# Kernel tuning notes

Hardware: AMD Instinct MI355X
Metric: run time of the kernel (lower is better)

## Reference

```python
import jax, jax.numpy as jnp
import numpy as np

B, T, EEG, GEO, TH, HID, OUT = 4096, 320, 64, 18, 32, 16, 4
THETA0, BETA, TAU_A, TAU_M, EPS = 0.5, 1.8, 0.36, 0.8, 1e-5


@jax.custom_vjp
def spike_fn(x):
    return jnp.where(x >= 0, 1.0, 0.0).astype(x.dtype)

def _spike_fwd(x):
    return spike_fn(x), x

def _spike_bwd(x, g):
    # SuperSpike-style surrogate gradient (original defvjp not shown in source)
    return (g / (10.0 * jnp.abs(x) + 1.0) ** 2,)

spike_fn.defvjp(_spike_fwd, _spike_bwd)


def setup_inputs() -> dict:
    key = jax.random.key(0)
    ks = jax.random.split(key, 20)
    rn = lambda k, s, sc=0.05: (jax.random.normal(k, s, jnp.float32) * sc)
    return {
        "x_eeg": jax.random.normal(ks[0], (B, T, EEG), jnp.float32),
        "x_geo": jax.random.normal(ks[1], (B, T, GEO), jnp.float32),
        "conv1_k": rn(ks[2], (5, EEG, TH)),   # (W, Cin, Cout)
        "conv1_b": jnp.zeros((TH,), jnp.float32),
        "bn1_scale": jnp.ones((TH,), jnp.float32),
        "bn1_bias": jnp.zeros((TH,), jnp.float32),
        "bn1_mean": rn(ks[3], (TH,)),
        "bn1_var": jnp.abs(rn(ks[4], (TH,))) + 1.0,
        "conv2_k": rn(ks[5], (3, TH, HID)),
        "conv2_b": jnp.zeros((HID,), jnp.float32),
        "bn2_scale": jnp.ones((HID,), jnp.float32),
        "bn2_bias": jnp.zeros((HID,), jnp.float32),
        "bn2_mean": rn(ks[6], (HID,)),
        "bn2_var": jnp.abs(rn(ks[7], (HID,))) + 1.0,
        "geo_W": rn(ks[8], (GEO, HID), 0.2),
        "geo_b": jnp.zeros((HID,), jnp.float32),
        "gamma": jnp.full((HID,), 0.5, jnp.float32),
        "fc1_W": rn(ks[9], (HID * 10, 64), 0.1),
        "fc1_b": jnp.zeros((64,), jnp.float32),
        "fc2_W": rn(ks[10], (64, OUT), 0.1),
        "fc2_b": jnp.zeros((OUT,), jnp.float32),
    }


def _conv1d(x, k, b, pad):
    # x: (B,T,C) NWC; k: (W,Cin,Cout) WIO
    return jax.lax.conv_general_dilated(
        x, k, window_strides=(1,), padding=[(pad, pad)],
        dimension_numbers=("NWC", "WIO", "NWC")) + b


def _bn(x, scale, bias, mean, var):
    return (x - mean) * jax.lax.rsqrt(var + EPS) * scale + bias


def reference(x_eeg, x_geo, conv1_k, conv1_b, bn1_scale, bn1_bias, bn1_mean,
              bn1_var, conv2_k, conv2_b, bn2_scale, bn2_bias, bn2_mean,
              bn2_var, geo_W, geo_b, gamma, fc1_W, fc1_b, fc2_W, fc2_b):
    x = jax.nn.relu(_bn(_conv1d(x_eeg, conv1_k, conv1_b, 2),
                        bn1_scale, bn1_bias, bn1_mean, bn1_var))
    eeg_encoded = jax.nn.relu(_bn(_conv1d(x, conv2_k, conv2_b, 1),
                                  bn2_scale, bn2_bias, bn2_mean, bn2_var))  # (B,T,HID)
    geo_mod = jax.nn.sigmoid(x_geo @ geo_W + geo_b)  # (B,T,HID)

    def scan_fn(carry, inputs):
        mem_alif, eta, mem_li, prev_spike = carry
        cur_eeg, cur_geo = inputs
        eta = TAU_A * eta + (1.0 - TAU_A) * prev_spike
        theta_t = THETA0 + BETA * eta - gamma * cur_geo
        mem_alif = TAU_M * mem_alif + cur_eeg
        spk = spike_fn(mem_alif - theta_t)
        mem_alif = mem_alif * (1.0 - spk)
        mem_li = 0.9 * mem_li + spk
        return (mem_alif, eta, mem_li, spk), mem_li

    z = jnp.zeros((B, HID), jnp.float32)
    _, mem_li_seq = jax.lax.scan(
        scan_fn, (z, z, z, z),
        (jnp.swapaxes(eeg_encoded, 0, 1), jnp.swapaxes(geo_mod, 0, 1)))
    mem_li_seq = jnp.swapaxes(jnp.swapaxes(mem_li_seq, 0, 1), 1, 2)  # (B,HID,T)

    windows = mem_li_seq.reshape(B, HID, 10, 32)
    dp_feat = (jnp.mean(windows[..., 16:], axis=-1) -
               jnp.mean(windows[..., :16], axis=-1)).reshape(B, -1)  # (B,160)
    out = jax.nn.relu(dp_feat @ fc1_W + fc1_b)
    return out @ fc2_W + fc2_b
```

## Files before the change

kernel.cpp:

```cpp
#include <hip/hip_runtime.h>

typedef _Float16 f16;
typedef __attribute__((ext_vector_type(8))) _Float16 f16x8;
typedef __attribute__((ext_vector_type(16))) float f32x16;

#define T_LEN 320

__device__ __forceinline__ void split2h(float v, unsigned short &h, unsigned short &l) {
    f16 hh = (f16)v;
    f16 ll = (f16)((v - (float)hh) * 4096.0f);
    h = __builtin_bit_cast(unsigned short, hh);
    l = __builtin_bit_cast(unsigned short, ll);
}

__global__ __launch_bounds__(256) void geo_prep_kernel(
    const float* __restrict__ k1, const float* __restrict__ c1b,
    const float* __restrict__ bn1s, const float* __restrict__ bn1b,
    const float* __restrict__ bn1m, const float* __restrict__ bn1v,
    const float* __restrict__ k2, const float* __restrict__ c2b,
    const float* __restrict__ bn2s, const float* __restrict__ bn2b,
    const float* __restrict__ bn2m, const float* __restrict__ bn2v,
    unsigned short* __restrict__ w1f, unsigned short* __restrict__ w2f,
    float* __restrict__ sb)
{
    const int tid = threadIdx.x;
    for (int e = tid; e < 20 * 64; e += 256) {
        const int ks = e >> 6, l = e & 63;
        const int lh = l >> 5, n = l & 31;
        for (int j = 0; j < 8; ++j) {
            const int kg = ks * 16 + lh * 8 + j;
            unsigned short h, lo; split2h(k1[kg * 32 + n], h, lo);
            w1f[((ks * 2 + 0) * 64 + l) * 8 + j] = h;
            w1f[((ks * 2 + 1) * 64 + l) * 8 + j] = lo;
        }
    }
    for (int e = tid; e < 6 * 64; e += 256) {
        const int ks = e >> 6, l = e & 63;
        const int lh = l >> 5, n = l & 31;
        for (int j = 0; j < 8; ++j) {
            const int kg = ks * 16 + lh * 8 + j;
            const float v = (n < 16) ? k2[kg * 16 + n] : 0.0f;
            unsigned short h, lo; split2h(v, h, lo);
            w2f[((ks * 2 + 0) * 64 + l) * 8 + j] = h;
            w2f[((ks * 2 + 1) * 64 + l) * 8 + j] = lo;
        }
    }
    if (tid < 32) {
        const float s1 = bn1s[tid] * (1.0f / sqrtf(bn1v[tid] + 1e-5f));
        sb[tid]      = s1;
        sb[32 + tid] = bn1b[tid] + (c1b[tid] - bn1m[tid]) * s1;
    }
    if (tid < 16) {
        const float s2 = bn2s[tid] * (1.0f / sqrtf(bn2v[tid] + 1e-5f));
        sb[64 + tid] = s2;
        sb[80 + tid] = bn2b[tid] + (c2b[tid] - bn2m[tid]) * s2;
    }
}

struct ConvSmem {
    unsigned short xh[70][64], xl[70][64];
    unsigned short c1h[66][40], c1l[66][40];
};

#define MFMA32(A, B, C) __builtin_amdgcn_mfma_f32_32x32x16_f16((A), (B), (C), 0, 0, 0)

__global__ __launch_bounds__(256, 5) void geo_alif_conv_kernel(
    const float* __restrict__ x_eeg,
    const unsigned short* __restrict__ w1f, const unsigned short* __restrict__ w2f,
    const float* __restrict__ sb, float* __restrict__ e_ws)
{
    __shared__ ConvSmem sm;
    const int tid = threadIdx.x, lane = tid & 63, wv = tid >> 6;
    const int l31 = lane & 31, lh = lane >> 5;
    const int row = blockIdx.x / 5, cc = blockIdx.x % 5;
    const int t0 = cc * 64;
    const float* xrow = x_eeg + (size_t)row * (T_LEN * 64);
    float* erow = e_ws + (size_t)row * (16 * T_LEN);

    {
        float4 v[5];
#pragma unroll
        for (int q = 0; q < 5; ++q) {
            const int fi = tid + q * 256;
            float4 tv = {0.f, 0.f, 0.f, 0.f};
            if (fi < 1120) {
                const int s = fi >> 4;
                const int tabs = t0 - 3 + s;
                if (tabs >= 0 && tabs < T_LEN)
                    tv = *reinterpret_cast<const float4*>(xrow + (size_t)tabs * 64 + (fi & 15) * 4);
            }
            v[q] = tv;
        }
#pragma unroll
        for (int q = 0; q < 5; ++q) {
            const int fi = tid + q * 256;
            if (fi < 1120) {
                const int s = fi >> 4, cq = fi & 15;
                unsigned short h0,l0,h1,l1,h2,l2,h3,l3;
                split2h(v[q].x, h0, l0); split2h(v[q].y, h1, l1);
                split2h(v[q].z, h2, l2); split2h(v[q].w, h3, l3);
                const int off = (((cq >> 1) ^ (s & 7)) * 8) + (cq & 1) * 4;
                ushort4 hv = {h0, h1, h2, h3}, lv = {l0, l1, l2, l3};
                *reinterpret_cast<ushort4*>(&sm.xh[s][off]) = hv;
                *reinterpret_cast<ushort4*>(&sm.xl[s][off]) = lv;
            }
        }
    }
    __syncthreads();

    if (wv < 3) {
        const int frag = wv;
        const float s1 = sb[l31], b1 = sb[32 + l31];
        const f16x8* w1v = reinterpret_cast<const f16x8*>(w1f);
        f32x16 am, cx;
#pragma unroll
        for (int q = 0; q < 16; ++q) { am[q] = 0.f; cx[q] = 0.f; }
        f16x8 pbh[4], pbl[4], pah[3], pal[3];
#pragma unroll
        for (int p = 0; p < 4; ++p) {
            pbh[p] = w1v[(p * 2 + 0) * 64 + lane];
            pbl[p] = w1v[(p * 2 + 1) * 64 + lane];
        }
#pragma unroll
        for (int p = 0; p < 3; ++p) {
            const int kb = p * 16 + lh * 8;
            int s = frag * 32 + l31 + (kb >> 6); if (s > 69) s = 69;
            const int off = ((((kb & 63) >> 3) ^ (s & 7)) * 8);
            pah[p] = *reinterpret_cast<const f16x8*>(&sm.xh[s][off]);
            pal[p] = *reinterpret_cast<const f16x8*>(&sm.xl[s][off]);
        }
#pragma unroll
        for (int ks = 0; ks < 20; ++ks) {
            const f16x8 ah = pah[ks % 3], al = pal[ks % 3];
            const f16x8 bh = pbh[ks % 4], bl = pbl[ks % 4];
            am = MFMA32(ah, bh, am);
            cx = MFMA32(ah, bl, cx);
            cx = MFMA32(al, bh, cx);
            if (ks < 17) {
                const int kb = (ks + 3) * 16 + lh * 8;
                int s = frag * 32 + l31 + (kb >> 6); if (s > 69) s = 69;
                const int off = ((((kb & 63) >> 3) ^ (s & 7)) * 8);
                pah[ks % 3] = *reinterpret_cast<const f16x8*>(&sm.xh[s][off]);
                pal[ks % 3] = *reinterpret_cast<const f16x8*>(&sm.xl[s][off]);
            }
            if (ks < 16) {
                pbh[ks % 4] = w1v[((ks + 4) * 2 + 0) * 64 + lane];
                pbl[ks % 4] = w1v[((ks + 4) * 2 + 1) * 64 + lane];
            }
        }
#pragma unroll
        for (int reg = 0; reg < 16; ++reg) {
            const int rl = frag * 32 + (reg & 3) + 8 * (reg >> 2) + 4 * lh;
            if (rl < 66) {
                const int tabs = t0 - 1 + rl;
                float v = am[reg] + cx[reg] * (1.0f / 4096.0f);
                v = (tabs >= 0 && tabs < T_LEN) ? fmaxf(v * s1 + b1, 0.0f) : 0.0f;
                unsigned short h_, lo_; split2h(v, h_, lo_);
                const int ui = (((l31 >> 3) ^ (rl & 3)) * 8) + (l31 & 7);
                sm.c1h[rl][ui] = h_;
                sm.c1l[rl][ui] = lo_;
            }
        }
    }
    __syncthreads();

    if (wv < 2) {
        const int mf = wv;
        const float s2 = (l31 < 16) ? sb[64 + l31] : 0.0f;
        const float b2 = (l31 < 16) ? sb[80 + l31] : 0.0f;
        const f16x8* w2v = reinterpret_cast<const f16x8*>(w2f);
        f16x8 w2hv[6], w2lv[6];
#pragma unroll
        for (int p = 0; p < 6; ++p) {
            w2hv[p] = w2v[(p * 2 + 0) * 64 + lane];
            w2lv[p] = w2v[(p * 2 + 1) * 64 + lane];
        }
        f32x16 am, cx;
#pragma unroll
        for (int q = 0; q < 16; ++q) { am[q] = 0.f; cx[q] = 0.f; }
#pragma unroll
        for (int ks = 0; ks < 6; ++ks) {
            const int kb = ks * 16 + lh * 8;
            const int sidx = mf * 32 + l31 + (kb >> 5);
            const int off = ((((kb & 31) >> 3) ^ (sidx & 3)) * 8);
            f16x8 ah = *reinterpret_cast<const f16x8*>(&sm.c1h[sidx][off]);
            f16x8 al = *reinterpret_cast<const f16x8*>(&sm.c1l[sidx][off]);
            am = MFMA32(ah, w2hv[ks], am);
            cx = MFMA32(ah, w2lv[ks], cx);
            cx = MFMA32(al, w2hv[ks], cx);
        }
        if (l31 < 16) {
#pragma unroll
            for (int g = 0; g < 4; ++g) {
                const int t = t0 + mf * 32 + 8 * g + 4 * lh;
                float4 ov;
                ov.x = fmaxf((am[g*4+0] + cx[g*4+0] * (1.0f/4096.0f)) * s2 + b2, 0.0f);
                ov.y = fmaxf((am[g*4+1] + cx[g*4+1] * (1.0f/4096.0f)) * s2 + b2, 0.0f);
                ov.z = fmaxf((am[g*4+2] + cx[g*4+2] * (1.0f/4096.0f)) * s2 + b2, 0.0f);
                ov.w = fmaxf((am[g*4+3] + cx[g*4+3] * (1.0f/4096.0f)) * s2 + b2, 0.0f);
                *reinterpret_cast<float4*>(erow + (size_t)l31 * T_LEN + t) = ov;
            }
        }
    }
}

__device__ __forceinline__ void loadxg18(float* d, const float* __restrict__ p) {
#pragma unroll
    for (int q = 0; q < 9; ++q) {
        float2 v = *reinterpret_cast<const float2*>(p + q * 2);
        d[q * 2]     = v.x;
        d[q * 2 + 1] = v.y;
    }
}

__global__ __launch_bounds__(256) void geo_alif_scan_kernel(
    const float* __restrict__ e_ws, const float* __restrict__ x_geo,
    const float* __restrict__ geoW, const float* __restrict__ geob,
    const float* __restrict__ gam,
    const float* __restrict__ fc1W, const float* __restrict__ fc1b,
    const float* __restrict__ fc2W, const float* __restrict__ fc2b,
    float* __restrict__ out)
{
    __shared__ float gW[19][16];
    __shared__ float geo_s[16][16][16];
    __shared__ float dp[16][160];
    __shared__ float h1s[16][64];

    const int tid = threadIdx.x;
    for (int i = tid; i < 288; i += 256) gW[i / 16][i & 15] = geoW[i];
    if (tid < 16) gW[18][tid] = geob[tid];
    __syncthreads();

    const int r = tid >> 4, h = tid & 15;
    const int b = blockIdx.x * 16 + r;
    const float* ep = e_ws + ((size_t)b * 16 + h) * T_LEN;
    const float gmv = gam[h];

    const int rg = tid >> 4, tl = tid & 15;
    const float* xgbase = x_geo + ((size_t)(blockIdx.x * 16 + rg) * T_LEN + tl) * 18;

    float xv[18];
    loadxg18(xv, xgbase);

    float mem = 0.f, eta = 0.f, li = 0.f, prev = 0.f, acc = 0.f;

    for (int c = 0; c < 20; ++c) {
        float nx[18];
        if (c < 19) loadxg18(nx, xgbase + (size_t)(c + 1) * 16 * 18);

        const float* ec = ep + c * 16;
        float4 ev0 = *reinterpret_cast<const float4*>(ec);
        float4 ev1 = *reinterpret_cast<const float4*>(ec + 4);
        float4 ev2 = *reinterpret_cast<const float4*>(ec + 8);
        float4 ev3 = *reinterpret_cast<const float4*>(ec + 12);

#pragma unroll
        for (int hh = 0; hh < 16; ++hh) {
            float a = gW[18][hh];
#pragma unroll
            for (int i = 0; i < 18; ++i) a = fmaf(xv[i], gW[i][hh], a);
            geo_s[rg][tl][hh] = 1.f / (1.f + expf(-a));
        }
        __syncthreads();

        float evs[16] = {ev0.x, ev0.y, ev0.z, ev0.w, ev1.x, ev1.y, ev1.z, ev1.w,
                         ev2.x, ev2.y, ev2.z, ev2.w, ev3.x, ev3.y, ev3.z, ev3.w};
#pragma unroll
        for (int u = 0; u < 16; ++u) {
            const int tt = c * 16 + u;
            const float g = geo_s[r][u][h];
            eta = 0.36f * eta + 0.64f * prev;
            const float th = 0.5f + 1.8f * eta - gmv * g;
            mem = 0.8f * mem + evs[u];
            const bool sp = (mem >= th);
            const float spk = sp ? 1.f : 0.f;
            prev = spk;
            mem = sp ? 0.f : mem;
            li = 0.9f * li + spk;
            acc += ((tt & 31) < 16) ? -li : li;
            if ((tt & 31) == 31) {
                dp[r][h * 10 + (tt >> 5)] = acc * 0.0625f;
                acc = 0.f;
            }
        }
        __syncthreads();

#pragma unroll
        for (int i = 0; i < 18; ++i) xv[i] = nx[i];
    }

    {
        const int rr = tid >> 4, j0 = tid & 15;
        float a0 = fc1b[j0], a1 = fc1b[j0 + 16], a2 = fc1b[j0 + 32], a3 = fc1b[j0 + 48];
        for (int f = 0; f < 160; ++f) {
            const float d = dp[rr][f];
            a0 = fmaf(d, fc1W[f * 64 + j0],      a0);
            a1 = fmaf(d, fc1W[f * 64 + j0 + 16], a1);
            a2 = fmaf(d, fc1W[f * 64 + j0 + 32], a2);
            a3 = fmaf(d, fc1W[f * 64 + j0 + 48], a3);
        }
        h1s[rr][j0]      = fmaxf(a0, 0.f);
        h1s[rr][j0 + 16] = fmaxf(a1, 0.f);
        h1s[rr][j0 + 32] = fmaxf(a2, 0.f);
        h1s[rr][j0 + 48] = fmaxf(a3, 0.f);
    }
    __syncthreads();

    if (tid < 64) {
        const int rr = tid >> 2, o = tid & 3;
        float a = fc2b[o];
#pragma unroll
        for (int j = 0; j < 64; ++j) a = fmaf(h1s[rr][j], fc2W[j * 4 + o], a);
        out[((size_t)(blockIdx.x * 16 + rr)) * 4 + o] = a;
    }
}

extern "C" void kernel_launch(void* const* d_in, const int* in_sizes, int n_in,
                              void* d_out, int out_size, void* d_ws, size_t ws_size,
                              hipStream_t stream) {
    (void)in_sizes; (void)n_in; (void)out_size; (void)ws_size;
    const float* x_eeg = (const float*)d_in[0];
    const float* x_geo = (const float*)d_in[1];
    const float* k1    = (const float*)d_in[2];
    const float* c1b   = (const float*)d_in[3];
    const float* bn1s  = (const float*)d_in[4];
    const float* bn1b  = (const float*)d_in[5];
    const float* bn1m  = (const float*)d_in[6];
    const float* bn1v  = (const float*)d_in[7];
    const float* k2    = (const float*)d_in[8];
    const float* c2b   = (const float*)d_in[9];
    const float* bn2s  = (const float*)d_in[10];
    const float* bn2b  = (const float*)d_in[11];
    const float* bn2m  = (const float*)d_in[12];
    const float* bn2v  = (const float*)d_in[13];
    const float* geoW  = (const float*)d_in[14];
    const float* geob  = (const float*)d_in[15];
    const float* gam   = (const float*)d_in[16];
    const float* fc1W  = (const float*)d_in[17];
    const float* fc1b  = (const float*)d_in[18];
    const float* fc2W  = (const float*)d_in[19];
    const float* fc2b  = (const float*)d_in[20];

    char* wsb = (char*)d_ws;
    unsigned short* w1f = (unsigned short*)(wsb);
    unsigned short* w2f = (unsigned short*)(wsb + 40960);
    float* sb           = (float*)(wsb + 53248);
    float* e_ws         = (float*)(wsb + 65536);

    geo_prep_kernel<<<1, 256, 0, stream>>>(
        k1, c1b, bn1s, bn1b, bn1m, bn1v,
        k2, c2b, bn2s, bn2b, bn2m, bn2v, w1f, w2f, sb);

    geo_alif_conv_kernel<<<4096 * 5, 256, 0, stream>>>(x_eeg, w1f, w2f, sb, e_ws);

    geo_alif_scan_kernel<<<256, 256, 0, stream>>>(
        e_ws, x_geo, geoW, geob, gam, fc1W, fc1b, fc2W, fc2b, (float*)d_out);
}
```

Before: 285.3 us.

## Move geo gate sigmoid computation into conv kernel as extra blocks

Adds 1024 extra blocks to the conv kernel that compute sigmoid(x_geo·W+b) for all batch rows and timesteps and store the result in a workspace buffer. The scan kernel then reads the precomputed gate instead of computing the geo projection inline, which shortens the latency-bound serial scan that runs on only 256 blocks. The cost is an extra 84 MB write and read of the gate tensor. A fallback keeps the old scan when the workspace is too small.

```diff
diff --git a/kernel.cpp b/kernel.cpp
--- a/kernel.cpp
+++ b/kernel.cpp
@@ -5,12 +5,22 @@
 typedef __attribute__((ext_vector_type(16))) float f32x16;
 
 #define T_LEN 320
+#define NGATE_BLOCKS 1024
 
 __device__ __forceinline__ void split2h(float v, unsigned short &h, unsigned short &l) {
     f16 hh = (f16)v;
     f16 ll = (f16)((v - (float)hh) * 4096.0f);
     h = __builtin_bit_cast(unsigned short, hh);
     l = __builtin_bit_cast(unsigned short, ll);
+}
+
+__device__ __forceinline__ void loadxg18(float* d, const float* __restrict__ p) {
+#pragma unroll
+    for (int q = 0; q < 9; ++q) {
+        float2 v = *reinterpret_cast<const float2*>(p + q * 2);
+        d[q * 2]     = v.x;
+        d[q * 2 + 1] = v.y;
+    }
 }
 
 __global__ __launch_bounds__(256) void geo_prep_kernel(
@@ -67,12 +77,38 @@
 __global__ __launch_bounds__(256, 5) void geo_alif_conv_kernel(
     const float* __restrict__ x_eeg,
     const unsigned short* __restrict__ w1f, const unsigned short* __restrict__ w2f,
-    const float* __restrict__ sb, float* __restrict__ e_ws)
+    const float* __restrict__ sb, float* __restrict__ e_ws,
+    const float* __restrict__ x_geo, const float* __restrict__ geoW,
+    const float* __restrict__ geob, float* __restrict__ g_ws, int ngate)
 {
     __shared__ ConvSmem sm;
+    __shared__ float gWs[19][16];
     const int tid = threadIdx.x, lane = tid & 63, wv = tid >> 6;
     const int l31 = lane & 31, lh = lane >> 5;
-    const int row = blockIdx.x / 5, cc = blockIdx.x % 5;
+
+    if (blockIdx.x < (unsigned)ngate) {
+        for (int i = tid; i < 288; i += 256) gWs[i / 16][i & 15] = geoW[i];
+        if (tid < 16) gWs[18][tid] = geob[tid];
+        __syncthreads();
+        for (int task = wv; task < 20; task += 4) {
+            const int rr = task / 5, seg = task - rr * 5;
+            const size_t gr = (size_t)blockIdx.x * 4 + rr;
+            const int t = seg * 64 + lane;
+            float xv[18];
+            loadxg18(xv, x_geo + (gr * T_LEN + t) * 18);
+#pragma unroll
+            for (int hh = 0; hh < 16; ++hh) {
+                float a = gWs[18][hh];
+#pragma unroll
+                for (int i = 0; i < 18; ++i) a = fmaf(xv[i], gWs[i][hh], a);
+                g_ws[(gr * 16 + hh) * T_LEN + t] = 1.f / (1.f + expf(-a));
+            }
+        }
+        return;
+    }
+
+    const int bid = blockIdx.x - ngate;
+    const int row = bid / 5, cc = bid % 5;
     const int t0 = cc * 64;
     const float* xrow = x_eeg + (size_t)row * (T_LEN * 64);
     float* erow = e_ws + (size_t)row * (16 * T_LEN);
@@ -204,16 +240,94 @@
     }
 }
 
-__device__ __forceinline__ void loadxg18(float* d, const float* __restrict__ p) {
-#pragma unroll
-    for (int q = 0; q < 9; ++q) {
-        float2 v = *reinterpret_cast<const float2*>(p + q * 2);
-        d[q * 2]     = v.x;
-        d[q * 2 + 1] = v.y;
-    }
-}
-
-__global__ __launch_bounds__(256) void geo_alif_scan_kernel(
+__global__ __launch_bounds__(256) void geo_alif_scan_pg(
+    const float* __restrict__ e_ws, const float* __restrict__ g_ws,
+    const float* __restrict__ gam,
+    const float* __restrict__ fc1W, const float* __restrict__ fc1b,
+    const float* __restrict__ fc2W, const float* __restrict__ fc2b,
+    float* __restrict__ out)
+{
+    __shared__ float dp[16][160];
+    __shared__ float h1s[16][64];
+
+    const int tid = threadIdx.x;
+    const int r = tid >> 4, h = tid & 15;
+    const int b = blockIdx.x * 16 + r;
+    const float* ep = e_ws + ((size_t)b * 16 + h) * T_LEN;
+    const float* gp = g_ws + ((size_t)b * 16 + h) * T_LEN;
+    const float gmv = gam[h];
+
+    float mem = 0.f, eta = 0.f, li = 0.f, prev = 0.f, acc = 0.f;
+
+    float4 ce[4], cg[4];
+#pragma unroll
+    for (int q = 0; q < 4; ++q) {
+        ce[q] = *reinterpret_cast<const float4*>(ep + q * 4);
+        cg[q] = *reinterpret_cast<const float4*>(gp + q * 4);
+    }
+
+    for (int c = 0; c < 20; ++c) {
+        float4 ne[4], ng[4];
+        if (c < 19) {
+#pragma unroll
+            for (int q = 0; q < 4; ++q) {
+                ne[q] = *reinterpret_cast<const float4*>(ep + (c + 1) * 16 + q * 4);
+                ng[q] = *reinterpret_cast<const float4*>(gp + (c + 1) * 16 + q * 4);
+            }
+        }
+        float evs[16] = {ce[0].x, ce[0].y, ce[0].z, ce[0].w, ce[1].x, ce[1].y, ce[1].z, ce[1].w,
+                         ce[2].x, ce[2].y, ce[2].z, ce[2].w, ce[3].x, ce[3].y, ce[3].z, ce[3].w};
+        float gvs[16] = {cg[0].x, cg[0].y, cg[0].z, cg[0].w, cg[1].x, cg[1].y, cg[1].z, cg[1].w,
+                         cg[2].x, cg[2].y, cg[2].z, cg[2].w, cg[3].x, cg[3].y, cg[3].z, cg[3].w};
+#pragma unroll
+        for (int u = 0; u < 16; ++u) {
+            const int tt = c * 16 + u;
+            eta = 0.36f * eta + 0.64f * prev;
+            const float th = 0.5f + 1.8f * eta - gmv * gvs[u];
+            mem = 0.8f * mem + evs[u];
+            const bool sp = (mem >= th);
+            const float spk = sp ? 1.f : 0.f;
+            prev = spk;
+            mem = sp ? 0.f : mem;
+            li = 0.9f * li + spk;
+            acc += ((tt & 31) < 16) ? -li : li;
+            if ((tt & 31) == 31) {
+                dp[r][h * 10 + (tt >> 5)] = acc * 0.0625f;
+                acc = 0.f;
+            }
+        }
+#pragma unroll
+        for (int q = 0; q < 4; ++q) { ce[q] = ne[q]; cg[q] = ng[q]; }
+    }
+    __syncthreads();
+
+    {
+        const int rr = tid >> 4, j0 = tid & 15;
+        float a0 = fc1b[j0], a1 = fc1b[j0 + 16], a2 = fc1b[j0 + 32], a3 = fc1b[j0 + 48];
+        for (int f = 0; f < 160; ++f) {
+            const float d = dp[rr][f];
+            a0 = fmaf(d, fc1W[f * 64 + j0],      a0);
+            a1 = fmaf(d, fc1W[f * 64 + j0 + 16], a1);
+            a2 = fmaf(d, fc1W[f * 64 + j0 + 32], a2);
+            a3 = fmaf(d, fc1W[f * 64 + j0 + 48], a3);
+        }
+        h1s[rr][j0]      = fmaxf(a0, 0.f);
+        h1s[rr][j0 + 16] = fmaxf(a1, 0.f);
+        h1s[rr][j0 + 32] = fmaxf(a2, 0.f);
+        h1s[rr][j0 + 48] = fmaxf(a3, 0.f);
+    }
+    __syncthreads();
+
+    if (tid < 64) {
+        const int rr = tid >> 2, o = tid & 3;
+        float a = fc2b[o];
+#pragma unroll
+        for (int j = 0; j < 64; ++j) a = fmaf(h1s[rr][j], fc2W[j * 4 + o], a);
+        out[((size_t)(blockIdx.x * 16 + rr)) * 4 + o] = a;
+    }
+}
+
+__global__ __launch_bounds__(256) void geo_alif_scan_fb(
     const float* __restrict__ e_ws, const float* __restrict__ x_geo,
     const float* __restrict__ geoW, const float* __restrict__ geob,
     const float* __restrict__ gam,
@@ -318,7 +432,7 @@
 extern "C" void kernel_launch(void* const* d_in, const int* in_sizes, int n_in,
                               void* d_out, int out_size, void* d_ws, size_t ws_size,
                               hipStream_t stream) {
-    (void)in_sizes; (void)n_in; (void)out_size; (void)ws_size;
+    (void)in_sizes; (void)n_in; (void)out_size;
     const float* x_eeg = (const float*)d_in[0];
     const float* x_geo = (const float*)d_in[1];
     const float* k1    = (const float*)d_in[2];
@@ -341,18 +455,29 @@
     const float* fc2W  = (const float*)d_in[19];
     const float* fc2b  = (const float*)d_in[20];
 
+    const size_t E_BYTES = (size_t)4096 * 16 * T_LEN * 4;
+    const size_t WS_NEEDED = 65536 + 2 * E_BYTES;
     char* wsb = (char*)d_ws;
     unsigned short* w1f = (unsigned short*)(wsb);
     unsigned short* w2f = (unsigned short*)(wsb + 40960);
     float* sb           = (float*)(wsb + 53248);
     float* e_ws         = (float*)(wsb + 65536);
 
+    const bool split_gate = (ws_size >= WS_NEEDED);
+    float* g_ws = split_gate ? (float*)(wsb + 65536 + E_BYTES) : nullptr;
+    const int ngate = split_gate ? NGATE_BLOCKS : 0;
+
     geo_prep_kernel<<<1, 256, 0, stream>>>(
         k1, c1b, bn1s, bn1b, bn1m, bn1v,
         k2, c2b, bn2s, bn2b, bn2m, bn2v, w1f, w2f, sb);
 
-    geo_alif_conv_kernel<<<4096 * 5, 256, 0, stream>>>(x_eeg, w1f, w2f, sb, e_ws);
-
-    geo_alif_scan_kernel<<<256, 256, 0, stream>>>(
-        e_ws, x_geo, geoW, geob, gam, fc1W, fc1b, fc2W, fc2b, (float*)d_out);
-}
+    geo_alif_conv_kernel<<<ngate + 4096 * 5, 256, 0, stream>>>(
+        x_eeg, w1f, w2f, sb, e_ws, x_geo, geoW, geob, g_ws, ngate);
+
+    if (split_gate)
+        geo_alif_scan_pg<<<256, 256, 0, stream>>>(
+            e_ws, g_ws, gam, fc1W, fc1b, fc2W, fc2b, (float*)d_out);
+    else
+        geo_alif_scan_fb<<<256, 256, 0, stream>>>(
+            e_ws, x_geo, geoW, geob, gam, fc1W, fc1b, fc2W, fc2b, (float*)d_out);
+}
```

Result: slower. 645.1 us (+126.1%).
